# Kernel tuning notes

Measured on AMD Instinct MI355X. Metric: run time of the kernel, lower is better.

The kernel has to match this reference:

```python
import jax, jax.numpy as jnp
import numpy as np

N = 50_000          # nodes
E = 1_600_000       # edges (avg degree 32)
S_IN, V_IN = 128, 16
S_OUT, V_OUT = 128, 16
HID = max(V_IN, V_OUT)   # bottleneck=1 -> hidden = max(v_in, v_out)
SVO = 3                  # scalarization_vectorization_output_dim
EPS = 1e-8               # safe_norm eps


def setup_inputs() -> dict:
    key = jax.random.key(0)
    ks = jax.random.split(key, 12)
    scale = 0.05
    return {
        "scalar": jax.random.normal(ks[0], (N, S_IN), jnp.float32),
        "vector": jax.random.normal(ks[1], (N, V_IN, 3), jnp.float32),
        "edge_index": jax.random.randint(ks[2], (2, E), 0, N, jnp.int32),
        "frames": jax.random.normal(ks[3], (E, 3, 3), jnp.float32),
        # parameters (torch Linear convention: W has shape (out, in))
        "W_down": jax.random.normal(ks[4], (HID, V_IN), jnp.float32) * scale,
        "W_df": jax.random.normal(ks[5], (SVO, V_IN), jnp.float32) * scale,
        "W_so": jax.random.normal(ks[6], (S_OUT, HID + S_IN + 3 * SVO), jnp.float32) * scale,
        "b_so": jax.random.normal(ks[7], (S_OUT,), jnp.float32) * scale,
        "W_up": jax.random.normal(ks[8], (V_OUT, HID), jnp.float32) * scale,
        "W_g": jax.random.normal(ks[9], (V_OUT, S_OUT), jnp.float32) * scale,
        "b_g": jax.random.normal(ks[10], (V_OUT,), jnp.float32) * scale,
    }


def _scalarize(vdf, edge_index, frames, dim_size):
    # vdf: (N, 3xyz, SVO) node-wise down-projected vectors.
    # Gather source-node vectors per edge, rotate into each edge's local frame,
    # then scatter-mean back to source nodes (node_inputs=True path).
    row = edge_index[0]
    vi = vdf[row]                                    # (E, 3, SVO)
    local = jnp.einsum('eij,ejc->eic', frames, vi)   # project onto frame rows
    local = jnp.swapaxes(local, -1, -2).reshape(vi.shape[0], 3 * SVO)  # (E, 9)
    sums = jax.ops.segment_sum(local, row, num_segments=dim_size)
    cnt = jax.ops.segment_sum(jnp.ones((vi.shape[0],), local.dtype), row,
                              num_segments=dim_size)
    return sums / jnp.maximum(cnt, 1.0)[:, None]     # scatter mean, 0 for empty


def reference(scalar, vector, edge_index, frames,
              W_down, W_df, W_so, b_so, W_up, W_g, b_g):
    silu = jax.nn.silu
    v_pre = jnp.swapaxes(vector, -1, -2)             # (N, 3, V_IN)
    vh = v_pre @ W_down.T                            # (N, 3, HID) vector_down
    vnorm = jnp.sqrt(jnp.sum(vh * vh, axis=-2) + EPS)  # safe_norm over xyz -> (N, HID)
    vdf = v_pre @ W_df.T                             # (N, 3, SVO) vector_down_frames
    sh = _scalarize(vdf, edge_index, frames, scalar.shape[0])  # (N, 9)
    merged = jnp.concatenate([scalar, vnorm, sh], axis=-1)     # (N, S_IN+HID+9)
    s = merged @ W_so.T + b_so                       # (N, S_OUT) scalar_out
    # vector branch (vector_gate=True, frame_gate=False, no residual)
    vrep = jnp.swapaxes(vh @ W_up.T, -1, -2)         # (N, V_OUT, 3)
    gate = silu(s) @ W_g.T + b_g                     # (N, V_OUT)
    vrep = vrep * jax.nn.sigmoid(gate)[..., None]
    return silu(s), vrep
```

## Files before the change

kernel.cpp:

```cpp
#include <hip/hip_runtime.h>

typedef unsigned short ushort_t;
typedef __attribute__((ext_vector_type(4))) unsigned short bfx4;
typedef __attribute__((ext_vector_type(8))) unsigned short bfx8;
typedef __attribute__((ext_vector_type(8))) short sfx8;
typedef __attribute__((ext_vector_type(4))) float fx4;

#define NABLK  256
#define RTH    1024
#define KBMAX  52
#define CAPL   64
#define FLC    16
#define RD     6
#define QMAX   224

#define FXS 4194304.0f
#define FXONE (1 << 22)

__device__ __forceinline__ float bf2f(unsigned short u){
  unsigned int x = ((unsigned int)u) << 16;
  float f; __builtin_memcpy(&f, &x, 4); return f;
}
__device__ __forceinline__ unsigned short f2bf(float f){
  unsigned int x; __builtin_memcpy(&x, &f, 4);
  x += 0x7fffu + ((x >> 16) & 1u);
  return (unsigned short)(x >> 16);
}
__device__ __forceinline__ int f2fx(float v){ return __float2int_rn(v * FXS); }
__device__ __forceinline__ unsigned short f2h(float f){
  _Float16 h = (_Float16)f;
  unsigned short u; __builtin_memcpy(&u, &h, 2); return u;
}
__device__ __forceinline__ float h2f(unsigned int u16){
  unsigned short us = (unsigned short)u16;
  _Float16 h; __builtin_memcpy(&h, &us, 2); return (float)h;
}
__device__ __forceinline__ unsigned int pk2(float a, float b){
  return (unsigned int)f2h(a) | ((unsigned int)f2h(b) << 16);
}

__global__ void k_pack(const float* __restrict__ wso, ushort_t* __restrict__ wpk)
{
  int idx = blockIdx.x * 256 + threadIdx.x;
  if (idx >= 8*5*64*8) return;
  int j    = idx & 7;
  int lane = (idx >> 3) & 63;
  int ks   = (idx >> 9) % 5;
  int nt   = idx / 2560;
  int mrow = lane & 15, quad = lane >> 4;
  int o = nt*16 + mrow;
  int k = ks*32 + quad*8 + j;
  float v = (k < 153) ? wso[o*153 + k] : 0.f;
  wpk[idx] = f2bf(v);
}

__global__ void k_edge(const int* __restrict__ ei, const float* __restrict__ frames,
                       float* __restrict__ sums, int E)
{
  int e = blockIdx.x * 256 + threadIdx.x;
  if (e >= E) return;
  int row = ei[e];
  const float* fp = frames + (size_t)e * 9;
  float F[9];
  __builtin_memcpy(F, fp, 36);
  float* sp = sums + (size_t)row * 10;
  #pragma unroll
  for (int t = 0; t < 9; t++) atomicAdd(&sp[t], F[t]);
  atomicAdd(&sp[9], 1.0f);
}

__global__ __launch_bounds__(RTH) void k_part(const int* __restrict__ ei,
                                              const float* __restrict__ frames,
                                              unsigned int* __restrict__ recs,
                                              int* __restrict__ counts,
                                              float* __restrict__ sums,
                                              int E, int EPB, int KB, int CAPG)
{
  __shared__ unsigned int s_buf[KBMAX * CAPL * RD];
  __shared__ int s_cnt[KBMAX];
  __shared__ int s_gof[KBMAX];
  __shared__ int s_cap[KBMAX];
  __shared__ int s_qb[QMAX];
  __shared__ int s_qd[QMAX];
  __shared__ int s_nq;

  const int tid  = threadIdx.x;
  const int ablk = blockIdx.x;
  const int e0 = ablk * EPB;
  const int e1 = min(e0 + EPB, E);

  for (int b = tid; b < KB; b += RTH){ s_cnt[b] = 0; s_gof[b] = 0; s_cap[b] = CAPG; }
  if (tid == 0) s_nq = 0;
  __syncthreads();

  for (int i0 = e0; i0 < e1; i0 += RTH){
    int e = i0 + tid;
    if (e < e1){
      int row = ei[e];
      float F[9];
      __builtin_memcpy(F, frames + (size_t)e * 9, 36);
      int b   = row >> 10;
      int loc = row & 1023;
      int slot = atomicAdd(&s_cnt[b], 1);
      if (slot < CAPL){
        uint2* d2 = (uint2*)(s_buf + (b * CAPL + slot) * RD);
        d2[0] = make_uint2(pk2(F[0], F[1]), pk2(F[2], F[3]));
        d2[1] = make_uint2(pk2(F[4], F[5]), pk2(F[6], F[7]));
        d2[2] = make_uint2((unsigned int)f2h(F[8]) | ((unsigned int)loc << 16), 0u);
      } else {
        float* sp = sums + (size_t)row * 10;
        #pragma unroll
        for (int t = 0; t < 9; t++) atomicAdd(&sp[t], F[t]);
        atomicAdd(&sp[9], 1.0f);
      }
    }
    __syncthreads();
    if (tid < KB){
      int c = min(s_cnt[tid], CAPL);
      int nf = c >> 4;
      int rem = c & (FLC - 1);
      if (nf > 0){
        int off = s_gof[tid];
        s_gof[tid] = off + nf * FLC;
        for (int k = 0; k < nf; k++){
          int q = atomicAdd(&s_nq, 1);
          int doff = off + k * FLC;
          s_qb[q] = (tid << 8) | (rem + k * FLC);
          if (doff + FLC <= CAPG){
            s_qd[q] = doff;
          } else {
            s_qd[q] = -1;
            s_cap[tid] = min(s_cap[tid], doff);
          }
        }
        s_cnt[tid] = rem;
      }
    }
    __syncthreads();
    const int nq = s_nq;
    for (int i = tid; i < nq * (FLC * RD); i += RTH){
      int q = i / (FLC * RD), d = i - q * (FLC * RD);
      int doff = s_qd[q];
      if (doff >= 0){
        int bb = s_qb[q] >> 8, ss = s_qb[q] & 255;
        recs[((size_t)(bb * NABLK + ablk) * CAPG + doff) * RD + d] =
            s_buf[(bb * CAPL + ss) * RD + d];
      }
    }
    for (int i = tid; i < nq * FLC; i += RTH){
      int q = i / FLC, rr = i - q * FLC;
      if (s_qd[q] < 0){
        int bb = s_qb[q] >> 8, ss = (s_qb[q] & 255) + rr;
        const unsigned int* rp = s_buf + (bb * CAPL + ss) * RD;
        int loc = rp[4] >> 16;
        float* sp = sums + (size_t)((bb << 10) + loc) * 10;
        atomicAdd(&sp[0], h2f(rp[0] & 65535u)); atomicAdd(&sp[1], h2f(rp[0] >> 16));
        atomicAdd(&sp[2], h2f(rp[1] & 65535u)); atomicAdd(&sp[3], h2f(rp[1] >> 16));
        atomicAdd(&sp[4], h2f(rp[2] & 65535u)); atomicAdd(&sp[5], h2f(rp[2] >> 16));
        atomicAdd(&sp[6], h2f(rp[3] & 65535u)); atomicAdd(&sp[7], h2f(rp[3] >> 16));
        atomicAdd(&sp[8], h2f(rp[4] & 65535u)); atomicAdd(&sp[9], 1.0f);
      }
    }
    __syncthreads();
    if (tid == 0) s_nq = 0;
  }

  for (int i = tid; i < KB * FLC; i += RTH){
    int b = i / FLC, rec = i - b * FLC;
    if (rec < s_cnt[b]){
      int off = s_gof[b] + rec;
      const unsigned int* rp = s_buf + (b * CAPL + rec) * RD;
      if (off < s_cap[b]){
        uint2* dp = (uint2*)(recs + ((size_t)(b * NABLK + ablk) * CAPG + off) * RD);
        dp[0] = make_uint2(rp[0], rp[1]);
        dp[1] = make_uint2(rp[2], rp[3]);
        dp[2] = make_uint2(rp[4], rp[5]);
      } else {
        int loc = rp[4] >> 16;
        float* sp = sums + (size_t)((b << 10) + loc) * 10;
        atomicAdd(&sp[0], h2f(rp[0] & 65535u)); atomicAdd(&sp[1], h2f(rp[0] >> 16));
        atomicAdd(&sp[2], h2f(rp[1] & 65535u)); atomicAdd(&sp[3], h2f(rp[1] >> 16));
        atomicAdd(&sp[4], h2f(rp[2] & 65535u)); atomicAdd(&sp[5], h2f(rp[2] >> 16));
        atomicAdd(&sp[6], h2f(rp[3] & 65535u)); atomicAdd(&sp[7], h2f(rp[3] >> 16));
        atomicAdd(&sp[8], h2f(rp[4] & 65535u)); atomicAdd(&sp[9], 1.0f);
      }
    }
  }
  if (tid < KB)
    counts[tid * NABLK + ablk] = min(s_gof[tid] + s_cnt[tid], s_cap[tid]);
}

template <int SPN>
__global__ __launch_bounds__(256) void k_accum_t(const unsigned int* __restrict__ recs,
                                                 const int* __restrict__ counts,
                                                 float* __restrict__ part, int CAPG)
{
  constexpr int APS2 = NABLK / SPN;
  __shared__ int s_pref[APS2 + 1];
  __shared__ int s_acc[1024 * 11];
  const int bucket = blockIdx.x / SPN;
  const int sp     = blockIdx.x - bucket * SPN;
  const int tid    = threadIdx.x;

  if (tid < APS2) s_pref[tid + 1] = counts[bucket * NABLK + sp * APS2 + tid];
  if (tid == 0) s_pref[0] = 0;
  for (int i = tid; i < 1024 * 11; i += 256) s_acc[i] = 0;
  __syncthreads();
  #pragma unroll
  for (int off = 1; off < APS2; off <<= 1){
    int v = 0;
    if (tid < APS2 && tid + 1 > off) v = s_pref[tid + 1 - off];
    __syncthreads();
    if (tid < APS2) s_pref[tid + 1] += v;
    __syncthreads();
  }
  const int total = s_pref[APS2];

  for (int base = 0; base < total; base += 1024){
    int got[4]; size_t ra[4];
    #pragma unroll
    for (int u = 0; u < 4; u++){
      got[u] = 0; ra[u] = 0;
      int idx = base + u * 256 + tid;
      if (idx < total){
        int lo = 0, hi = APS2;
        while (hi - lo > 1){ int mid = (lo + hi) >> 1; if (s_pref[mid] <= idx) lo = mid; else hi = mid; }
        int slot = idx - s_pref[lo];
        int ablk = sp * APS2 + lo;
        ra[u] = ((size_t)(bucket * NABLK + ablk) * CAPG + slot);
        got[u] = 1;
      }
    }
    uint2 a0[4], a1[4], a2[4];
    #pragma unroll
    for (int u = 0; u < 4; u++){
      if (got[u]){
        const unsigned int* rp = recs + ra[u] * RD;
        a0[u] = *(const uint2*)(rp + 0);
        a1[u] = *(const uint2*)(rp + 2);
        a2[u] = *(const uint2*)(rp + 4);
      }
    }
    #pragma unroll
    for (int u = 0; u < 4; u++){
      if (got[u]){
        int loc = a2[u].x >> 16;
        int* ap = s_acc + loc * 11;
        atomicAdd(&ap[0], f2fx(h2f(a0[u].x & 65535u)));
        atomicAdd(&ap[1], f2fx(h2f(a0[u].x >> 16)));
        atomicAdd(&ap[2], f2fx(h2f(a0[u].y & 65535u)));
        atomicAdd(&ap[3], f2fx(h2f(a0[u].y >> 16)));
        atomicAdd(&ap[4], f2fx(h2f(a1[u].x & 65535u)));
        atomicAdd(&ap[5], f2fx(h2f(a1[u].x >> 16)));
        atomicAdd(&ap[6], f2fx(h2f(a1[u].y & 65535u)));
        atomicAdd(&ap[7], f2fx(h2f(a1[u].y >> 16)));
        atomicAdd(&ap[8], f2fx(h2f(a2[u].x & 65535u)));
        atomicAdd(&ap[9], FXONE);
      }
    }
  }
  __syncthreads();
  float* pb = part + (size_t)(bucket * SPN + sp) * 10240;
  for (int i = tid; i < 10240; i += 256)
    pb[i] = (float)s_acc[(i / 10) * 11 + (i % 10)] * (1.0f / FXS);
}

#define NPB 64
#define MS  168
#define WGS 136

template <int SPN>
__global__ __launch_bounds__(256) void k_node(
    const float* __restrict__ scalar, const float* __restrict__ vec,
    const float* __restrict__ sums,   const float* __restrict__ part,
    const float* __restrict__ wdown, const float* __restrict__ wdf,
    const ushort_t* __restrict__ wpk, const float* __restrict__ bso,
    const float* __restrict__ wup,   const float* __restrict__ wg,
    const float* __restrict__ bg,
    float* __restrict__ out0, float* __restrict__ out1, int N)
{
  __shared__ __align__(16) ushort_t sm_merged[NPB * MS];
  __shared__ __align__(16) ushort_t sm_vh[NPB * 48];
  __shared__ __align__(16) ushort_t sm_wg[16 * WGS];
  __shared__ __align__(16) ushort_t sm_wupb[512];
  __shared__ float  sm_sh[NPB * 10];
  __shared__ float  sm_vdf[NPB * 9];
  __shared__ float  sm_wd[256];
  __shared__ float  sm_wdf[48];
  __shared__ float  sm_bso[128];
  __shared__ float  sm_bg[16];

  const int tid = threadIdx.x;
  const int n0  = blockIdx.x * NPB;

  {
    int nv = N - n0; if (nv > NPB) nv = NPB;
    const int valid = nv * 48;
    fx4* scratch = (fx4*)sm_merged;
    for (int idx = tid; idx < NPB*48/4; idx += 256){
      fx4 val = {0.f, 0.f, 0.f, 0.f};
      if (idx*4 < valid) val = *(const fx4*)(vec + (size_t)n0*48 + idx*4);
      scratch[idx] = val;
    }
  }
  sm_wd[tid] = wdown[(tid & 15)*16 + (tid >> 4)];
  if (tid < 48) sm_wdf[tid] = wdf[tid];
  for (int idx = tid; idx < NPB*10; idx += 256){
    int ni = idx / 10, sl = idx - ni*10;
    int g = n0 + ni;
    float acc = 0.f;
    if (g < N){
      acc = sums[(size_t)g*10 + sl];
      if (part){
        int bucket = g >> 10, loc = g & 1023;
        const float* pb = part + (size_t)bucket * SPN * 10240 + loc * 10 + sl;
        #pragma unroll
        for (int sp = 0; sp < SPN; sp++) acc += pb[(size_t)sp * 10240];
      }
    }
    sm_sh[idx] = acc;
  }
  __syncthreads();

  #pragma unroll
  for (int it = 0; it < 4; it++){
    int idx = tid + it*256;
    int ni = idx >> 4, h = idx & 15;
    const float* sv = (const float*)sm_merged + ni*48;
    float a0 = 0.f, a1 = 0.f, a2 = 0.f;
    #pragma unroll
    for (int k = 0; k < 16; k++){
      float w = sm_wd[k*16 + h];
      a0 += sv[k*3+0]*w; a1 += sv[k*3+1]*w; a2 += sv[k*3+2]*w;
    }
    sm_vh[ni*48 +  0 + h] = f2bf(a0);
    sm_vh[ni*48 + 16 + h] = f2bf(a1);
    sm_vh[ni*48 + 32 + h] = f2bf(a2);
  }
  if (tid < NPB*3){
    const int ni = tid / 3, d = tid - ni*3;
    const float* sv = (const float*)sm_merged + ni*48;
    float c0 = 0.f, c1 = 0.f, c2 = 0.f;
    #pragma unroll
    for (int k = 0; k < 16; k++){
      float v = sv[k*3 + d];
      c0 += v * sm_wdf[ 0 + k];
      c1 += v * sm_wdf[16 + k];
      c2 += v * sm_wdf[32 + k];
    }
    sm_vdf[ni*9 + d*3 + 0] = c0;
    sm_vdf[ni*9 + d*3 + 1] = c1;
    sm_vdf[ni*9 + d*3 + 2] = c2;
  }
  __syncthreads();

  for (int idx = tid; idx < NPB*32; idx += 256){
    int ni = idx >> 5, c4 = (idx & 31) * 4;
    int g = n0 + ni;
    if (g < N){
      fx4 x = *(const fx4*)(scalar + (size_t)g*128 + c4);
      bfx4 b; b[0]=f2bf(x[0]); b[1]=f2bf(x[1]); b[2]=f2bf(x[2]); b[3]=f2bf(x[3]);
      *(bfx4*)(sm_merged + ni*MS + c4) = b;
    } else {
      bfx4 b = {0,0,0,0};
      *(bfx4*)(sm_merged + ni*MS + c4) = b;
    }
  }
  #pragma unroll
  for (int it = 0; it < 4; it++){
    int idx = tid + it*256;
    int ni = idx >> 4, h = idx & 15;
    float x0 = bf2f(sm_vh[ni*48 +  0 + h]);
    float x1 = bf2f(sm_vh[ni*48 + 16 + h]);
    float x2 = bf2f(sm_vh[ni*48 + 32 + h]);
    sm_merged[ni*MS + 128 + h] = f2bf(sqrtf(x0*x0 + x1*x1 + x2*x2 + 1e-8f));
  }
  for (int idx = tid; idx < NPB*9; idx += 256){
    int ni = idx / 9, t = idx - ni*9;
    int c = t / 3, i3 = (t - c*3) * 3;
    float cnt = sm_sh[ni*10 + 9];
    float inv = 1.0f / fmaxf(cnt, 1.0f);
    const float* Fs = sm_sh + ni*10;
    const float* vd = sm_vdf + ni*9;
    float val = Fs[i3+0]*vd[0*3+c] + Fs[i3+1]*vd[1*3+c] + Fs[i3+2]*vd[2*3+c];
    sm_merged[ni*MS + 144 + t] = f2bf(val * inv);
  }
  for (int idx = tid; idx < NPB*7; idx += 256){
    int ni = idx / 7, t = idx - ni*7;
    sm_merged[ni*MS + 153 + t] = 0;
  }
  for (int idx = tid; idx < 2048; idx += 256)
    sm_wg[(idx >> 7)*WGS + (idx & 127)] = f2bf(wg[idx]);
  {
    float w = wup[tid];
    unsigned short hi = f2bf(w);
    sm_wupb[tid]       = hi;
    sm_wupb[256 + tid] = f2bf(w - bf2f(hi));
  }
  if (tid < 128) sm_bso[tid] = bso[tid];
  if (tid < 16) sm_bg[tid] = bg[tid];
  __syncthreads();

  const int lane = tid & 63;
  const int wv   = tid >> 6;
  const int mrow = lane & 15;
  const int quad = lane >> 4;
  sfx8 afr[5];
  {
    const ushort_t* ab = sm_merged + (wv*16 + mrow)*MS + quad*8;
    #pragma unroll
    for (int ks = 0; ks < 5; ks++) afr[ks] = *(const sfx8*)(ab + ks*32);
  }
  const ushort_t* wb = wpk + lane*8;
  #pragma unroll
  for (int nt = 0; nt < 8; nt++){
    fx4 acc = {0.f, 0.f, 0.f, 0.f};
    #pragma unroll
    for (int ks = 0; ks < 5; ks++){
      sfx8 bfr = *(const sfx8*)(wb + (size_t)(nt*5 + ks)*64*8);
      acc = __builtin_amdgcn_mfma_f32_16x16x32_bf16(afr[ks], bfr, acc, 0, 0, 0);
    }
    const int o = nt*16 + mrow;
    const float bso_v = sm_bso[o];
    #pragma unroll
    for (int r = 0; r < 4; r++){
      int m = quad*4 + r;
      int g = n0 + wv*16 + m;
      float s = acc[r] + bso_v;
      float sact = s / (1.f + __expf(-s));
      if (g < N) out0[(size_t)g*128 + o] = sact;
      sm_merged[(wv*16 + m)*MS + o] = f2bf(sact);
    }
  }
  __syncthreads();

  {
    fx4 accg = {0.f, 0.f, 0.f, 0.f};
    const ushort_t* ga = sm_merged + (wv*16 + mrow)*MS + quad*8;
    const ushort_t* gb = sm_wg + mrow*WGS + quad*8;
    #pragma unroll
    for (int ks = 0; ks < 4; ks++){
      sfx8 af = *(const sfx8*)(ga + ks*32);
      sfx8 bf = *(const sfx8*)(gb + ks*32);
      accg = __builtin_amdgcn_mfma_f32_16x16x32_bf16(af, bf, accg, 0, 0, 0);
    }
    float sig[4];
    #pragma unroll
    for (int r = 0; r < 4; r++){
      float gv = accg[r] + sm_bg[mrow];
      sig[r] = 1.f / (1.f + __expf(-gv));
    }
    const sfx8 zero8 = {0,0,0,0,0,0,0,0};
    sfx8 bhi = zero8, blo = zero8;
    if (quad < 2){
      bhi = *(const sfx8*)(sm_wupb + mrow*16 + quad*8);
      blo = *(const sfx8*)(sm_wupb + 256 + mrow*16 + quad*8);
    }
    #pragma unroll
    for (int d = 0; d < 3; d++){
      sfx8 av = zero8;
      if (quad < 2)
        av = *(const sfx8*)(sm_vh + (wv*16 + mrow)*48 + d*16 + quad*8);
      fx4 accv = {0.f, 0.f, 0.f, 0.f};
      accv = __builtin_amdgcn_mfma_f32_16x16x32_bf16(av, blo, accv, 0, 0, 0);
      accv = __builtin_amdgcn_mfma_f32_16x16x32_bf16(av, bhi, accv, 0, 0, 0);
      #pragma unroll
      for (int r = 0; r < 4; r++){
        int m = quad*4 + r;
        int g = n0 + wv*16 + m;
        if (g < N) out1[((size_t)g*16 + mrow)*3 + d] = accv[r] * sig[r];
      }
    }
  }
}

extern "C" void kernel_launch(void* const* d_in, const int* in_sizes, int n_in,
                              void* d_out, int out_size, void* d_ws, size_t ws_size,
                              hipStream_t stream)
{
  const float* scalar = (const float*)d_in[0];
  const float* vec    = (const float*)d_in[1];
  const int*   ei     = (const int*)d_in[2];
  const float* frames = (const float*)d_in[3];
  const float* wdown  = (const float*)d_in[4];
  const float* wdf    = (const float*)d_in[5];
  const float* wso    = (const float*)d_in[6];
  const float* bso    = (const float*)d_in[7];
  const float* wup    = (const float*)d_in[8];
  const float* wg     = (const float*)d_in[9];
  const float* bg     = (const float*)d_in[10];

  const int N = in_sizes[0] / 128;
  const int E = in_sizes[2] / 2;
  const int KB  = (N + 1023) >> 10;
  const int EPB = (E + NABLK - 1) / NABLK;

  float lam = (float)EPB / (float)KB;
  int capg = (int)(lam + 3.5f * sqrtf(lam) + 17.0f);
  capg = (capg + 15) & ~15;

  char* wp = (char*)d_ws;
  float*        sums  = (float*)wp;                wp += (size_t)N * 10 * sizeof(float);
  ushort_t*     wpk   = (ushort_t*)wp;             wp += (size_t)8*5*64*8 * sizeof(ushort_t);
  int*          counts= (int*)wp;                  wp += (size_t)KB * NABLK * sizeof(int);
  unsigned int* recs  = (unsigned int*)wp;         wp += (size_t)KB * NABLK * capg * RD * sizeof(unsigned int);
  float*        part  = (float*)wp;
  const size_t base_need = (size_t)((char*)part - (char*)d_ws);
  const size_t need16 = base_need + (size_t)KB * 16 * 10240 * sizeof(float);
  const size_t need8  = base_need + (size_t)KB *  8 * 10240 * sizeof(float);

  float* out0 = (float*)d_out;
  float* out1 = out0 + (size_t)N * 128;

  int SPN = 0;
  if (KB <= KBMAX && E < (1 << 25)){
    if (ws_size >= need16) SPN = 16;
    else if (ws_size >= need8) SPN = 8;
  }

  (void)hipMemsetAsync(sums, 0, (size_t)N * 10 * sizeof(float), stream);
  k_pack<<<(8*5*64*8 + 255)/256, 256, 0, stream>>>(wso, wpk);
  if (SPN == 16){
    k_part<<<NABLK, RTH, 0, stream>>>(ei, frames, recs, counts, sums, E, EPB, KB, capg);
    k_accum_t<16><<<KB * 16, 256, 0, stream>>>(recs, counts, part, capg);
    k_node<16><<<(N + NPB - 1) / NPB, 256, 0, stream>>>(scalar, vec, sums, part,
                                                        wdown, wdf, wpk, bso, wup, wg, bg,
                                                        out0, out1, N);
  } else if (SPN == 8){
    k_part<<<NABLK, RTH, 0, stream>>>(ei, frames, recs, counts, sums, E, EPB, KB, capg);
    k_accum_t<8><<<KB * 8, 256, 0, stream>>>(recs, counts, part, capg);
    k_node<8><<<(N + NPB - 1) / NPB, 256, 0, stream>>>(scalar, vec, sums, part,
                                                       wdown, wdf, wpk, bso, wup, wg, bg,
                                                       out0, out1, N);
  } else {
    k_edge<<<(E + 255) / 256, 256, 0, stream>>>(ei, frames, sums, E);
    k_node<16><<<(N + NPB - 1) / NPB, 256, 0, stream>>>(scalar, vec, sums, nullptr,
                                                        wdown, wdf, wpk, bso, wup, wg, bg,
                                                        out0, out1, N);
  }
}
```

Before: 220.5 us.

## Fuse memset into weight pack, double edge partition blocks, keep partials integer

Replaces the separate memset of the per-node sums buffer and the weight-packing kernel with one prep kernel that does both, which saves a launch. It doubles NABLK so edge partitioning runs on 512 blocks, and each accumulation block now covers twice as many source partitions. Fixed-point partial sums are stored as ints and reduced in integer before a single conversion in the node kernel. This saves per-element float conversions and gives an exact reduction, but more blocks mean more counts, more record capacity and more prefix-scan work.

```diff
diff --git a/kernel.cpp b/kernel.cpp
--- a/kernel.cpp
+++ b/kernel.cpp
@@ -6,7 +6,7 @@
 typedef __attribute__((ext_vector_type(8))) short sfx8;
 typedef __attribute__((ext_vector_type(4))) float fx4;
 
-#define NABLK  256
+#define NABLK  512
 #define RTH    1024
 #define KBMAX  52
 #define CAPL   64
@@ -39,19 +39,29 @@
   return (unsigned int)f2h(a) | ((unsigned int)f2h(b) << 16);
 }
 
-__global__ void k_pack(const float* __restrict__ wso, ushort_t* __restrict__ wpk)
+__global__ __launch_bounds__(256) void k_prep(const float* __restrict__ wso,
+                                              ushort_t* __restrict__ wpk,
+                                              float* __restrict__ sums, int N10)
 {
-  int idx = blockIdx.x * 256 + threadIdx.x;
-  if (idx >= 8*5*64*8) return;
-  int j    = idx & 7;
-  int lane = (idx >> 3) & 63;
-  int ks   = (idx >> 9) % 5;
-  int nt   = idx / 2560;
-  int mrow = lane & 15, quad = lane >> 4;
-  int o = nt*16 + mrow;
-  int k = ks*32 + quad*8 + j;
-  float v = (k < 153) ? wso[o*153 + k] : 0.f;
-  wpk[idx] = f2bf(v);
+  int gid = blockIdx.x * 256 + threadIdx.x;
+  int b4 = gid * 4;
+  if (b4 + 4 <= N10){
+    fx4 z = {0.f, 0.f, 0.f, 0.f};
+    *(fx4*)(sums + b4) = z;
+  } else if (b4 < N10){
+    for (int t = b4; t < N10; t++) sums[t] = 0.f;
+  }
+  if (gid < 8*5*64*8){
+    int j    = gid & 7;
+    int lane = (gid >> 3) & 63;
+    int ks   = (gid >> 9) % 5;
+    int nt   = gid / 2560;
+    int mrow = lane & 15, quad = lane >> 4;
+    int o = nt*16 + mrow;
+    int k = ks*32 + quad*8 + j;
+    float v = (k < 153) ? wso[o*153 + k] : 0.f;
+    wpk[gid] = f2bf(v);
+  }
 }
 
 __global__ void k_edge(const int* __restrict__ ei, const float* __restrict__ frames,
@@ -193,7 +203,7 @@
 template <int SPN>
 __global__ __launch_bounds__(256) void k_accum_t(const unsigned int* __restrict__ recs,
                                                  const int* __restrict__ counts,
-                                                 float* __restrict__ part, int CAPG)
+                                                 int* __restrict__ part, int CAPG)
 {
   constexpr int APS2 = NABLK / SPN;
   __shared__ int s_pref[APS2 + 1];
@@ -260,9 +270,9 @@
     }
   }
   __syncthreads();
-  float* pb = part + (size_t)(bucket * SPN + sp) * 10240;
+  int* pb = part + (size_t)(bucket * SPN + sp) * 10240;
   for (int i = tid; i < 10240; i += 256)
-    pb[i] = (float)s_acc[(i / 10) * 11 + (i % 10)] * (1.0f / FXS);
+    pb[i] = s_acc[(i / 10) * 11 + (i % 10)];
 }
 
 #define NPB 64
@@ -272,7 +282,7 @@
 template <int SPN>
 __global__ __launch_bounds__(256) void k_node(
     const float* __restrict__ scalar, const float* __restrict__ vec,
-    const float* __restrict__ sums,   const float* __restrict__ part,
+    const float* __restrict__ sums,   const int* __restrict__ part,
     const float* __restrict__ wdown, const float* __restrict__ wdf,
     const ushort_t* __restrict__ wpk, const float* __restrict__ bso,
     const float* __restrict__ wup,   const float* __restrict__ wg,
@@ -313,9 +323,11 @@
       acc = sums[(size_t)g*10 + sl];
       if (part){
         int bucket = g >> 10, loc = g & 1023;
-        const float* pb = part + (size_t)bucket * SPN * 10240 + loc * 10 + sl;
+        const int* pb = part + (size_t)bucket * SPN * 10240 + loc * 10 + sl;
+        int ai = 0;
         #pragma unroll
-        for (int sp = 0; sp < SPN; sp++) acc += pb[(size_t)sp * 10240];
+        for (int sp = 0; sp < SPN; sp++) ai += pb[(size_t)sp * 10240];
+        acc += (float)ai * (1.0f / FXS);
       }
     }
     sm_sh[idx] = acc;
@@ -504,10 +516,10 @@
   ushort_t*     wpk   = (ushort_t*)wp;             wp += (size_t)8*5*64*8 * sizeof(ushort_t);
   int*          counts= (int*)wp;                  wp += (size_t)KB * NABLK * sizeof(int);
   unsigned int* recs  = (unsigned int*)wp;         wp += (size_t)KB * NABLK * capg * RD * sizeof(unsigned int);
-  float*        part  = (float*)wp;
+  int*          part  = (int*)wp;
   const size_t base_need = (size_t)((char*)part - (char*)d_ws);
-  const size_t need16 = base_need + (size_t)KB * 16 * 10240 * sizeof(float);
-  const size_t need8  = base_need + (size_t)KB *  8 * 10240 * sizeof(float);
+  const size_t need16 = base_need + (size_t)KB * 16 * 10240 * sizeof(int);
+  const size_t need8  = base_need + (size_t)KB *  8 * 10240 * sizeof(int);
 
   float* out0 = (float*)d_out;
   float* out1 = out0 + (size_t)N * 128;
@@ -518,8 +530,11 @@
     else if (ws_size >= need8) SPN = 8;
   }
 
-  (void)hipMemsetAsync(sums, 0, (size_t)N * 10 * sizeof(float), stream);
-  k_pack<<<(8*5*64*8 + 255)/256, 256, 0, stream>>>(wso, wpk);
+  const int N10 = N * 10;
+  int prepBlocks = ((N10 + 3) / 4 + 255) / 256;
+  if (prepBlocks < 80) prepBlocks = 80;
+  k_prep<<<prepBlocks, 256, 0, stream>>>(wso, wpk, sums, N10);
+
   if (SPN == 16){
     k_part<<<NABLK, RTH, 0, stream>>>(ei, frames, recs, counts, sums, E, EPB, KB, capg);
     k_accum_t<16><<<KB * 16, 256, 0, stream>>>(recs, counts, part, capg);
```

After: 222.9 us. About the same (+1.1%).
